# Kernel tuning notes

Hardware: AMD Instinct MI355X
Metric: run time of the kernel (lower is better)

Reference implementation:

```python
import jax, jax.numpy as jnp
import numpy as np

H = 1.0  # binarization scale (default in module)

def round_through(x):
    # straight-through estimator: forward = round(x), backward = identity
    return x + jax.lax.stop_gradient(jnp.round(x) - x)

def binary_tanh_unit(x):
    hs = jnp.clip((x + 1.0) / 2.0, 0.0, 1.0)  # hard sigmoid
    return 2.0 * round_through(hs) - 1.0

def setup_inputs() -> dict:
    key = jax.random.key(0)
    kx, kw, kb = jax.random.split(key, 3)
    N, d_in, d_out = 16384, 1024, 1024
    x = jax.random.normal(kx, (N, d_in), dtype=jnp.float32)
    # kernel initialized uniform in [-H, H] per the module
    W = jax.random.uniform(kw, (d_in, d_out), dtype=jnp.float32, minval=-H, maxval=H)
    b = jax.random.normal(kb, (d_out,), dtype=jnp.float32) * 0.01
    return {"x": x, "W": W, "b": b}

def reference(x, W, b):
    # binarize weights to +/-H, then dense matmul + bias
    Wb = H * binary_tanh_unit(W / H)  # values in {-H, +H}
    out = jnp.matmul(x, Wb) + b       # [N, d_out]
    return out
```

## Files before the change

### kernel.cpp

```cpp
#include <hip/hip_runtime.h>
#include <stdint.h>

typedef __bf16 bf16_t;
typedef __bf16 bf16x8 __attribute__((ext_vector_type(8)));
typedef float f32x4 __attribute__((ext_vector_type(4)));

#define M_DIM 16384
#define N_DIM 1024
#define K_DIM 1024
#define BM 128
#define BN 256
#define BK 32
#define NT (K_DIM / BK)
#define A_SLOT 16384
#define B_SLOT 16384
#define B_BASE 32768

__global__ void bin_transpose_w(const float* __restrict__ W,
                                unsigned short* __restrict__ WbT) {
    __shared__ unsigned short t[64][68];
    int tj = blockIdx.x;
    int ti = blockIdx.y;
    int tid = threadIdx.x;
    int c4 = (tid & 15) * 4;
    int r0 = tid >> 4;
#pragma unroll
    for (int p = 0; p < 4; ++p) {
        int r = r0 + p * 16;
        float4 v = *(const float4*)(W + (size_t)(ti * 64 + r) * N_DIM + tj * 64 + c4);
        t[r][c4 + 0] = ((v.x + 1.0f) * 0.5f > 0.5f) ? 0x3F80 : 0xBF80;
        t[r][c4 + 1] = ((v.y + 1.0f) * 0.5f > 0.5f) ? 0x3F80 : 0xBF80;
        t[r][c4 + 2] = ((v.z + 1.0f) * 0.5f > 0.5f) ? 0x3F80 : 0xBF80;
        t[r][c4 + 3] = ((v.w + 1.0f) * 0.5f > 0.5f) ? 0x3F80 : 0xBF80;
    }
    __syncthreads();
#pragma unroll
    for (int p = 0; p < 4; ++p) {
        int rn = r0 + p * 16;
        ushort4 o;
        o.x = t[c4 + 0][rn];
        o.y = t[c4 + 1][rn];
        o.z = t[c4 + 2][rn];
        o.w = t[c4 + 3][rn];
        *(ushort4*)(WbT + (size_t)(tj * 64 + rn) * K_DIM + ti * 64 + c4) = o;
    }
}

__device__ __forceinline__ void gload16(const void* g, const void* l) {
    __builtin_amdgcn_global_load_lds(
        (const __attribute__((address_space(1))) void*)(g),
        (__attribute__((address_space(3))) void*)(l),
        16, 0, 0);
}

__global__ __launch_bounds__(512, 4) void bgemm(const float* __restrict__ X,
                                                const bf16_t* __restrict__ Bt,
                                                const float* __restrict__ bias,
                                                float* __restrict__ C) {
    __shared__ __align__(16) char lds[2 * A_SLOT + 2 * B_SLOT];

    const int nwg = (M_DIM / BM) * (N_DIM / BN);
    int bid = blockIdx.x;
    int swz = (bid & 7) * (nwg >> 3) + (bid >> 3);
    int tile_n = swz & 3;
    int tile_m = swz >> 2;
    int bm0 = tile_m * BM;
    int bn0 = tile_n * BN;

    int tid = threadIdx.x;
    int w = tid >> 6, l = tid & 63;
    int wr = w >> 2, wc = w & 3;
    int lr = l & 15, lk = l >> 4;

    int arow = tid >> 3;
    int achk = (tid & 7) ^ (arow & 7);
    auto stageA = [&](int t, int c) {
        gload16(X + (size_t)(bm0 + c * 64 + arow) * K_DIM + t * BK + achk * 4,
                lds + (t & 1) * A_SLOT + c * 8192 + tid * 16);
    };
    int brow = tid >> 2;
    int bchk = (tid & 3) ^ ((brow >> 1) & 3);
    auto stageB = [&](int t, int c) {
        gload16(Bt + (size_t)(bn0 + c * 128 + brow) * K_DIM + t * BK + bchk * 8,
                lds + B_BASE + (t & 1) * B_SLOT + c * 8192 + tid * 16);
    };

    f32x4 acc[4][4];
#pragma unroll
    for (int m = 0; m < 4; ++m)
#pragma unroll
        for (int n = 0; n < 4; ++n)
            acc[m][n] = (f32x4)(0.0f);

    stageA(0, 0); stageA(0, 1); stageB(0, 0); stageB(0, 1);
    asm volatile("s_waitcnt vmcnt(0)" ::: "memory");
    __builtin_amdgcn_s_barrier();

    for (int t = 0; t < NT; ++t) {
        if (t + 1 < NT) {
            stageA(t + 1, 0); stageA(t + 1, 1);
            stageB(t + 1, 0); stageB(t + 1, 1);
        }

        const char* Ab = lds + (t & 1) * A_SLOT;
        const char* Bb = lds + B_BASE + (t & 1) * B_SLOT;

        bf16x8 bfr[4];
#pragma unroll
        for (int n = 0; n < 4; ++n) {
            int br = wc * 64 + n * 16 + lr;
            bfr[n] = *(const bf16x8*)(Bb + br * 64 + ((lk ^ ((br >> 1) & 3)) * 16));
        }
#pragma unroll
        for (int m = 0; m < 4; ++m) {
            int r = wr * 64 + m * 16 + lr;
            const char* rb = Ab + r * 128;
            float4 lo = *(const float4*)(rb + (((2 * lk) ^ (r & 7)) * 16));
            float4 hi = *(const float4*)(rb + (((2 * lk + 1) ^ (r & 7)) * 16));
            bf16x8 afr;
            afr[0] = (__bf16)lo.x; afr[1] = (__bf16)lo.y;
            afr[2] = (__bf16)lo.z; afr[3] = (__bf16)lo.w;
            afr[4] = (__bf16)hi.x; afr[5] = (__bf16)hi.y;
            afr[6] = (__bf16)hi.z; afr[7] = (__bf16)hi.w;
#pragma unroll
            for (int n = 0; n < 4; ++n)
                acc[m][n] = __builtin_amdgcn_mfma_f32_16x16x32_bf16(
                    afr, bfr[n], acc[m][n], 0, 0, 0);
        }

        if (t + 1 < NT) {
            asm volatile("s_waitcnt vmcnt(0)" ::: "memory");
            __builtin_amdgcn_s_barrier();
        }
    }

#pragma unroll
    for (int n = 0; n < 4; ++n) {
        int col = bn0 + wc * 64 + n * 16 + lr;
        float bv = bias[col];
#pragma unroll
        for (int m = 0; m < 4; ++m) {
            int row0 = bm0 + wr * 64 + m * 16 + lk * 4;
#pragma unroll
            for (int j = 0; j < 4; ++j)
                C[(size_t)(row0 + j) * N_DIM + col] = acc[m][n][j] + bv;
        }
    }
}

__global__ void naive_bin_dense(const float* __restrict__ x,
                                const float* __restrict__ W,
                                const float* __restrict__ b,
                                float* __restrict__ out) {
    int col = blockIdx.x * 256 + threadIdx.x;
    int row = blockIdx.y;
    float acc = 0.0f;
    for (int k = 0; k < K_DIM; ++k) {
        float s = ((W[(size_t)k * N_DIM + col] + 1.0f) * 0.5f > 0.5f) ? 1.0f : -1.0f;
        acc += x[(size_t)row * K_DIM + k] * s;
    }
    out[(size_t)row * N_DIM + col] = acc + b[col];
}

extern "C" void kernel_launch(void* const* d_in, const int* in_sizes, int n_in,
                              void* d_out, int out_size, void* d_ws, size_t ws_size,
                              hipStream_t stream) {
    const float* x = (const float*)d_in[0];
    const float* W = (const float*)d_in[1];
    const float* b = (const float*)d_in[2];
    float* out = (float*)d_out;

    size_t wb_bytes = (size_t)K_DIM * N_DIM * sizeof(unsigned short);

    if (ws_size >= wb_bytes) {
        unsigned short* wbt = (unsigned short*)d_ws;
        hipLaunchKernelGGL(bin_transpose_w, dim3(N_DIM / 64, K_DIM / 64), dim3(256),
                           0, stream, W, wbt);
        hipLaunchKernelGGL(bgemm, dim3((M_DIM / BM) * (N_DIM / BN)), dim3(512), 0, stream,
                           x, (const bf16_t*)wbt, b, out);
    } else {
        hipLaunchKernelGGL(naive_bin_dense, dim3(N_DIM / 256, M_DIM), dim3(256),
                           0, stream, x, W, b, out);
    }
}
```

Before: 54.89 us.

## Restructure GEMM: register-staged A conversion to bf16 LDS, B fragments direct from global

```diff
diff --git a/kernel.cpp b/kernel.cpp
--- a/kernel.cpp
+++ b/kernel.cpp
@@ -8,13 +8,11 @@
 #define M_DIM 16384
 #define N_DIM 1024
 #define K_DIM 1024
-#define BM 128
-#define BN 256
+#define BM 256
+#define BN 128
 #define BK 32
 #define NT (K_DIM / BK)
 #define A_SLOT 16384
-#define B_SLOT 16384
-#define B_BASE 32768
 
 __global__ void bin_transpose_w(const float* __restrict__ W,
                                 unsigned short* __restrict__ WbT) {
@@ -46,90 +44,98 @@
     }
 }
 
-__device__ __forceinline__ void gload16(const void* g, const void* l) {
-    __builtin_amdgcn_global_load_lds(
-        (const __attribute__((address_space(1))) void*)(g),
-        (__attribute__((address_space(3))) void*)(l),
-        16, 0, 0);
-}
-
-__global__ __launch_bounds__(512, 4) void bgemm(const float* __restrict__ X,
+__global__ __launch_bounds__(256, 2) void bgemm(const float* __restrict__ X,
                                                 const bf16_t* __restrict__ Bt,
                                                 const float* __restrict__ bias,
                                                 float* __restrict__ C) {
-    __shared__ __align__(16) char lds[2 * A_SLOT + 2 * B_SLOT];
+    __shared__ __align__(16) char lds[2 * A_SLOT];
 
     const int nwg = (M_DIM / BM) * (N_DIM / BN);
     int bid = blockIdx.x;
     int swz = (bid & 7) * (nwg >> 3) + (bid >> 3);
-    int tile_n = swz & 3;
-    int tile_m = swz >> 2;
+    int tile_m = swz >> 3;
+    int tile_n = swz & 7;
     int bm0 = tile_m * BM;
     int bn0 = tile_n * BN;
 
     int tid = threadIdx.x;
     int w = tid >> 6, l = tid & 63;
-    int wr = w >> 2, wc = w & 3;
+    int wr = w >> 1, wc = w & 1;
     int lr = l & 15, lk = l >> 4;
 
-    int arow = tid >> 3;
-    int achk = (tid & 7) ^ (arow & 7);
-    auto stageA = [&](int t, int c) {
-        gload16(X + (size_t)(bm0 + c * 64 + arow) * K_DIM + t * BK + achk * 4,
-                lds + (t & 1) * A_SLOT + c * 8192 + tid * 16);
-    };
-    int brow = tid >> 2;
-    int bchk = (tid & 3) ^ ((brow >> 1) & 3);
-    auto stageB = [&](int t, int c) {
-        gload16(Bt + (size_t)(bn0 + c * 128 + brow) * K_DIM + t * BK + bchk * 8,
-                lds + B_BASE + (t & 1) * B_SLOT + c * 8192 + tid * 16);
-    };
+    int ar = tid >> 2, ac = tid & 3;
+    const bf16_t* bbase = Bt + (size_t)(bn0 + wc * 64 + lr) * K_DIM + lk * 8;
 
-    f32x4 acc[4][4];
+    f32x4 acc[8][4];
 #pragma unroll
-    for (int m = 0; m < 4; ++m)
+    for (int m = 0; m < 8; ++m)
 #pragma unroll
         for (int n = 0; n < 4; ++n)
             acc[m][n] = (f32x4)(0.0f);
 
-    stageA(0, 0); stageA(0, 1); stageB(0, 0); stageB(0, 1);
-    asm volatile("s_waitcnt vmcnt(0)" ::: "memory");
+    float4 a_st[4][2];
+    bf16x8 b_act[4], b_st[4];
+
+    auto loadA = [&](int t) {
+#pragma unroll
+        for (int p = 0; p < 4; ++p) {
+            const float4* s = (const float4*)(X + (size_t)(bm0 + ar + 64 * p) * K_DIM
+                                              + t * BK + ac * 8);
+            a_st[p][0] = s[0];
+            a_st[p][1] = s[1];
+        }
+    };
+    auto loadB = [&](int t, bf16x8* d) {
+#pragma unroll
+        for (int n = 0; n < 4; ++n)
+            d[n] = *(const bf16x8*)(bbase + (size_t)n * 16 * K_DIM + t * BK);
+    };
+    auto writeA = [&](int t) {
+#pragma unroll
+        for (int p = 0; p < 4; ++p) {
+            bf16x8 v;
+            v[0] = (__bf16)a_st[p][0].x; v[1] = (__bf16)a_st[p][0].y;
+            v[2] = (__bf16)a_st[p][0].z; v[3] = (__bf16)a_st[p][0].w;
+            v[4] = (__bf16)a_st[p][1].x; v[5] = (__bf16)a_st[p][1].y;
+            v[6] = (__bf16)a_st[p][1].z; v[7] = (__bf16)a_st[p][1].w;
+            int r = ar + 64 * p;
+            *(bf16x8*)(lds + (t & 1) * A_SLOT + r * 64
+                       + ((ac ^ ((r >> 1) & 3)) * 16)) = v;
+        }
+    };
+
+    loadA(0);
+    loadB(0, b_act);
+    writeA(0);
+    loadA(1);
+    loadB(1, b_st);
+    asm volatile("s_waitcnt lgkmcnt(0)" ::: "memory");
+    __builtin_amdgcn_sched_barrier(0);
     __builtin_amdgcn_s_barrier();
 
     for (int t = 0; t < NT; ++t) {
-        if (t + 1 < NT) {
-            stageA(t + 1, 0); stageA(t + 1, 1);
-            stageB(t + 1, 0); stageB(t + 1, 1);
-        }
+        const char* Ab = lds + (t & 1) * A_SLOT;
 
-        const char* Ab = lds + (t & 1) * A_SLOT;
-        const char* Bb = lds + B_BASE + (t & 1) * B_SLOT;
-
-        bf16x8 bfr[4];
 #pragma unroll
-        for (int n = 0; n < 4; ++n) {
-            int br = wc * 64 + n * 16 + lr;
-            bfr[n] = *(const bf16x8*)(Bb + br * 64 + ((lk ^ ((br >> 1) & 3)) * 16));
-        }
-#pragma unroll
-        for (int m = 0; m < 4; ++m) {
-            int r = wr * 64 + m * 16 + lr;
-            const char* rb = Ab + r * 128;
-            float4 lo = *(const float4*)(rb + (((2 * lk) ^ (r & 7)) * 16));
-            float4 hi = *(const float4*)(rb + (((2 * lk + 1) ^ (r & 7)) * 16));
-            bf16x8 afr;
-            afr[0] = (__bf16)lo.x; afr[1] = (__bf16)lo.y;
-            afr[2] = (__bf16)lo.z; afr[3] = (__bf16)lo.w;
-            afr[4] = (__bf16)hi.x; afr[5] = (__bf16)hi.y;
-            afr[6] = (__bf16)hi.z; afr[7] = (__bf16)hi.w;
+        for (int m = 0; m < 8; ++m) {
+            int r = wr * 128 + m * 16 + lr;
+            bf16x8 afr = *(const bf16x8*)(Ab + r * 64 + ((lk ^ ((r >> 1) & 3)) * 16));
 #pragma unroll
             for (int n = 0; n < 4; ++n)
                 acc[m][n] = __builtin_amdgcn_mfma_f32_16x16x32_bf16(
-                    afr, bfr[n], acc[m][n], 0, 0, 0);
+                    afr, b_act[n], acc[m][n], 0, 0, 0);
         }
 
         if (t + 1 < NT) {
-            asm volatile("s_waitcnt vmcnt(0)" ::: "memory");
+            writeA(t + 1);
+#pragma unroll
+            for (int n = 0; n < 4; ++n) b_act[n] = b_st[n];
+            if (t + 2 < NT) {
+                loadA(t + 2);
+                loadB(t + 2, b_st);
+            }
+            asm volatile("s_waitcnt lgkmcnt(0)" ::: "memory");
+            __builtin_amdgcn_sched_barrier(0);
             __builtin_amdgcn_s_barrier();
         }
     }
@@ -139,8 +145,8 @@
         int col = bn0 + wc * 64 + n * 16 + lr;
         float bv = bias[col];
 #pragma unroll
-        for (int m = 0; m < 4; ++m) {
-            int row0 = bm0 + wr * 64 + m * 16 + lk * 4;
+        for (int m = 0; m < 8; ++m) {
+            int row0 = bm0 + wr * 128 + m * 16 + lk * 4;
 #pragma unroll
             for (int j = 0; j < 4; ++j)
                 C[(size_t)(row0 + j) * N_DIM + col] = acc[m][n][j] + bv;
@@ -176,7 +182,7 @@
         unsigned short* wbt = (unsigned short*)d_ws;
         hipLaunchKernelGGL(bin_transpose_w, dim3(N_DIM / 64, K_DIM / 64), dim3(256),
                            0, stream, W, wbt);
-        hipLaunchKernelGGL(bgemm, dim3((M_DIM / BM) * (N_DIM / BN)), dim3(512), 0, stream,
+        hipLaunchKernelGGL(bgemm, dim3((M_DIM / BM) * (N_DIM / BN)), dim3(256), 0, stream,
                            x, (const bf16_t*)wbt, b, out);
     } else {
         hipLaunchKernelGGL(naive_bin_dense, dim3(N_DIM / 256, M_DIM), dim3(256),
```

Measured after the change: 66.05 us. +20.3%, slower.

## Stage A tile through registers and convert to bf16 before LDS write

Applied to the files above, without the earlier changes.

```diff
diff --git a/kernel.cpp b/kernel.cpp
--- a/kernel.cpp
+++ b/kernel.cpp
@@ -12,9 +12,9 @@
 #define BN 256
 #define BK 32
 #define NT (K_DIM / BK)
-#define A_SLOT 16384
+#define A_SLOT 8192
 #define B_SLOT 16384
-#define B_BASE 32768
+#define B_BASE 16384
 
 __global__ void bin_transpose_w(const float* __restrict__ W,
                                 unsigned short* __restrict__ WbT) {
@@ -72,12 +72,23 @@
     int wr = w >> 2, wc = w & 3;
     int lr = l & 15, lk = l >> 4;
 
-    int arow = tid >> 3;
-    int achk = (tid & 7) ^ (arow & 7);
-    auto stageA = [&](int t, int c) {
-        gload16(X + (size_t)(bm0 + c * 64 + arow) * K_DIM + t * BK + achk * 4,
-                lds + (t & 1) * A_SLOT + c * 8192 + tid * 16);
+    int ar = tid >> 2, ac = tid & 3;
+    int aslot = ac ^ ((ar >> 1) & 3);
+    const float* asrc = X + (size_t)(bm0 + ar) * K_DIM + ac * 8;
+    float4 a_lo, a_hi;
+    auto loadA = [&](int t) {
+        const float4* s = (const float4*)(asrc + t * BK);
+        a_lo = s[0]; a_hi = s[1];
     };
+    auto writeA = [&](int t) {
+        bf16x8 v;
+        v[0] = (__bf16)a_lo.x; v[1] = (__bf16)a_lo.y;
+        v[2] = (__bf16)a_lo.z; v[3] = (__bf16)a_lo.w;
+        v[4] = (__bf16)a_hi.x; v[5] = (__bf16)a_hi.y;
+        v[6] = (__bf16)a_hi.z; v[7] = (__bf16)a_hi.w;
+        *(bf16x8*)(lds + (t & 1) * A_SLOT + ar * 64 + aslot * 16) = v;
+    };
+
     int brow = tid >> 2;
     int bchk = (tid & 3) ^ ((brow >> 1) & 3);
     auto stageB = [&](int t, int c) {
@@ -92,13 +103,16 @@
         for (int n = 0; n < 4; ++n)
             acc[m][n] = (f32x4)(0.0f);
 
-    stageA(0, 0); stageA(0, 1); stageB(0, 0); stageB(0, 1);
+    loadA(0);
+    stageB(0, 0); stageB(0, 1);
     asm volatile("s_waitcnt vmcnt(0)" ::: "memory");
+    writeA(0);
+    asm volatile("s_waitcnt lgkmcnt(0)" ::: "memory");
     __builtin_amdgcn_s_barrier();
 
     for (int t = 0; t < NT; ++t) {
         if (t + 1 < NT) {
-            stageA(t + 1, 0); stageA(t + 1, 1);
+            loadA(t + 1);
             stageB(t + 1, 0); stageB(t + 1, 1);
         }
 
@@ -114,14 +128,7 @@
 #pragma unroll
         for (int m = 0; m < 4; ++m) {
             int r = wr * 64 + m * 16 + lr;
-            const char* rb = Ab + r * 128;
-            float4 lo = *(const float4*)(rb + (((2 * lk) ^ (r & 7)) * 16));
-            float4 hi = *(const float4*)(rb + (((2 * lk + 1) ^ (r & 7)) * 16));
-            bf16x8 afr;
-            afr[0] = (__bf16)lo.x; afr[1] = (__bf16)lo.y;
-            afr[2] = (__bf16)lo.z; afr[3] = (__bf16)lo.w;
-            afr[4] = (__bf16)hi.x; afr[5] = (__bf16)hi.y;
-            afr[6] = (__bf16)hi.z; afr[7] = (__bf16)hi.w;
+            bf16x8 afr = *(const bf16x8*)(Ab + r * 64 + ((lk ^ ((r >> 1) & 3)) * 16));
 #pragma unroll
             for (int n = 0; n < 4; ++n)
                 acc[m][n] = __builtin_amdgcn_mfma_f32_16x16x32_bf16(
@@ -130,6 +137,8 @@
 
         if (t + 1 < NT) {
             asm volatile("s_waitcnt vmcnt(0)" ::: "memory");
+            writeA(t + 1);
+            asm volatile("s_waitcnt lgkmcnt(0)" ::: "memory");
             __builtin_amdgcn_s_barrier();
         }
     }
```

Measured after the change: 72.07 us. 1.31x slower.
